# Kernel tuning notes

Measured on AMD Instinct MI355X. Metric: run time of the kernel, lower is better.

The kernel has to match this reference:

```python
import jax, jax.numpy as jnp
import numpy as np

SIGMA = 16
P = 2 * SIGMA + 1  # 33x33 patch
OUT = 128          # feature_extractor.output_size
DN = ('NCHW', 'OIHW', 'NCHW')


def setup_inputs() -> dict:
    key = jax.random.key(0)
    ks = jax.random.split(key, 10)
    B, K, H, W = 4, 64, 256, 256
    images_ground = jax.random.normal(ks[0], (B, 3, H, W), jnp.float32)
    images_satellite = jax.random.normal(ks[1], (B, 3, H, W), jnp.float32)
    # normalized keypoints kept in interior so sigma-window crops stay in-bounds
    keypoints_ground = 0.2 + 0.6 * jax.random.uniform(ks[2], (B, K, 2), jnp.float32)
    keypoints_satellite = 0.2 + 0.6 * jax.random.uniform(ks[3], (B, K, 2), jnp.float32)
    # small CNN feature extractor params (conv 3->32 s1, conv 32->64 s2, GAP, linear 64->OUT)
    w1 = jax.random.normal(ks[4], (32, 3, 3, 3), jnp.float32) * 0.1
    b1 = jnp.zeros((32,), jnp.float32)
    w2 = jax.random.normal(ks[5], (64, 32, 3, 3), jnp.float32) * 0.05
    b2 = jnp.zeros((64,), jnp.float32)
    wl = jax.random.normal(ks[6], (OUT, 64), jnp.float32) * 0.1
    bl = jnp.zeros((OUT,), jnp.float32)
    return dict(images_ground=images_ground, images_satellite=images_satellite,
                keypoints_ground=keypoints_ground, keypoints_satellite=keypoints_satellite,
                w1=w1, b1=b1, w2=w2, b2=b2, wl=wl, bl=bl, num_samples=K)


def _cnn(x, w1, b1, w2, b2, wl, bl):
    # x: [M, 3, P, P] -> [M, OUT]
    h = jax.lax.conv_general_dilated(x, w1, (1, 1), 'VALID', dimension_numbers=DN)
    h = jax.nn.relu(h + b1[None, :, None, None])
    h = jax.lax.conv_general_dilated(h, w2, (2, 2), 'VALID', dimension_numbers=DN)
    h = jax.nn.relu(h + b2[None, :, None, None])
    h = h.mean(axis=(2, 3))  # global average pool -> [M, 64]
    return h @ wl.T + bl


def _crop_all(images, kps_px):
    # images: [B,3,H,W]; kps_px: [N,2] pixel (x, y) coords -> patches [N,B,3,P,P]
    B = images.shape[0]
    hw = images.shape[-1]
    starts = jnp.clip(jnp.floor(kps_px).astype(jnp.int32) - SIGMA, 0, hw - P)
    def one(st):
        return jax.lax.dynamic_slice(images, (0, 0, st[1], st[0]), (B, 3, P, P))
    return jax.vmap(one)(starts)


def reference(images_ground, images_satellite, keypoints_ground, keypoints_satellite,
              w1, b1, w2, b2, wl, bl, num_samples):
    kg = (keypoints_ground * images_ground.shape[-1]).reshape(-1, 2)   # [N,2]
    ksat = (keypoints_satellite * images_satellite.shape[-1]).reshape(-1, 2)
    pg = _crop_all(images_ground, kg)        # [N,B,3,P,P]
    ps = _crop_all(images_satellite, ksat)   # [N,B,3,P,P]
    N, B = pg.shape[0], pg.shape[1]
    fg = _cnn(pg.reshape(N * B, 3, P, P), w1, b1, w2, b2, wl, bl)
    fs = _cnn(ps.reshape(N * B, 3, P, P), w1, b1, w2, b2, wl, bl)
    fg = fg.reshape(N, B, OUT).transpose(1, 0, 2)  # features_ground [B,N,OUT]
    fs = fs.reshape(N, B, OUT).transpose(1, 0, 2)
    return jnp.mean((fg - fs) ** 2)
```

## Files before the change

kernel.cpp:

```cpp
#include <hip/hip_runtime.h>

#define HW   256
#define Pp   33
#define PPAD 36
#define OUTF 128
#define SIG  16

#define KCP   40
#define PLROW (2 * 16 * KCP)
#define PLSZ  (6 * PLROW)
#define IMS   40

#define WS_W1FH 0
#define WS_W1FL 512
#define WS_BHI  1024
#define WS_BLO  10240
#define WS_WLT  19456

typedef __attribute__((ext_vector_type(8))) short v8s;
typedef __attribute__((ext_vector_type(4))) float f32x4;

__device__ __forceinline__ unsigned short f2bf_rne(float x) {
  unsigned u = __float_as_uint(x);
  unsigned r = (u + 0x7FFFu + ((u >> 16) & 1u)) >> 16;
  return (unsigned short)r;
}
__device__ __forceinline__ float bf2f(unsigned short h) {
  return __uint_as_float(((unsigned)h) << 16);
}

__global__ __launch_bounds__(256) void prep_kernel(
    const float* __restrict__ w1, const float* __restrict__ w2,
    const float* __restrict__ wl, float* __restrict__ ws,
    float* __restrict__ out) {
  int t = blockIdx.x * 256 + threadIdx.x;
  int stride = gridDim.x * 256;
  if (blockIdx.x == 0 && threadIdx.x == 0) out[0] = 0.0f;
  unsigned short* w1h = (unsigned short*)(ws + WS_W1FH);
  unsigned short* w1lo = (unsigned short*)(ws + WS_W1FL);
  for (int i = t; i < 1024; i += stride) {
    int j  = i & 7;
    int l  = (i >> 3) & 63;
    int nt = i >> 9;
    int k  = 8 * (l >> 4) + j;
    int ch = 16 * nt + (l & 15);
    float v = (k < 27) ? w1[ch * 27 + k] : 0.0f;
    unsigned short h = f2bf_rne(v);
    w1h[i]  = h;
    w1lo[i] = f2bf_rne(v - bf2f(h));
  }
  unsigned short* bhi = (unsigned short*)(ws + WS_BHI);
  unsigned short* blo = (unsigned short*)(ws + WS_BLO);
  for (int i = t; i < 18432; i += stride) {
    int j  = i & 7;
    int l  = (i >> 3) & 63;
    int w  = (i >> 9) & 3;
    int tp = i >> 11;
    int ch = w * 16 + (l & 15);
    int kc = ((l >> 4) << 3) + j;
    int ky = tp / 3, kx = tp - ky * 3;
    float v = w2[ch * 288 + kc * 9 + ky * 3 + kx];
    unsigned short h = f2bf_rne(v);
    bhi[i] = h;
    blo[i] = f2bf_rne(v - bf2f(h));
  }
  for (int i = t; i < 8192; i += stride) {
    int o = i & 127, ii = i >> 7;
    ws[WS_WLT + i] = wl[o * 64 + ii];
  }
}

__global__ __launch_bounds__(256) void patch_cnn_kernel(
    const float* __restrict__ imgG, const float* __restrict__ imgS,
    const float* __restrict__ kpG,  const float* __restrict__ kpS,
    const float* __restrict__ b1g,  const float* __restrict__ b2g,
    const float* __restrict__ blg,  const float* __restrict__ ws,
    float* __restrict__ out) {
  __shared__ __align__(16) unsigned short patch[3 * Pp * PPAD];
  __shared__ __align__(16) unsigned short imcol[2][32 * IMS];
  __shared__ __align__(16) unsigned short hiP[PLSZ];
  __shared__ float gapv[64];
  __shared__ float fstash[OUTF];
  __shared__ float lred[4];

  const int bid  = blockIdx.x;
  const int n    = bid >> 2;
  const int b    = bid & 3;
  const int tid  = threadIdx.x;
  const int wave = tid >> 6;
  const int lane = tid & 63;

  const int m16 = lane & 15;
  const int qq  = lane >> 4;
  const int mt  = wave & 1;
  const int nt  = wave >> 1;

  const int bm = tid & 31;
  const int kq = tid >> 5;
  int  boff[4];
  bool bval[4];
#pragma unroll
  for (int j = 0; j < 4; ++j) {
    int k = 4 * kq + j;
    bval[j] = (k < 27);
    int kk = bval[j] ? k : 0;
    int ci = kk / 9, r2 = kk - ci * 9, ky = r2 / 3, kx = r2 - ky * 3;
    boff[j] = (ci * Pp + ky) * PPAD + bm + kx;
  }

  const v8s w1hF = ((const v8s*)((const unsigned short*)(ws + WS_W1FH)))[nt * 64 + lane];
  const v8s w1lF = ((const v8s*)((const unsigned short*)(ws + WS_W1FL)))[nt * 64 + lane];
  const float b1v = b1g[nt * 16 + m16];

  const v8s* bhW = (const v8s*)((const unsigned short*)(ws + WS_BHI)) + (wave * 64 + lane);
  const v8s* blW = (const v8s*)((const unsigned short*)(ws + WS_BLO)) + (wave * 64 + lane);
  const float b2v = b2g[wave * 16 + m16];

  auto build_row = [&](int r, int ibuf) {
    unsigned short h[4];
#pragma unroll
    for (int j = 0; j < 4; ++j)
      h[j] = bval[j] ? patch[boff[j] + r * PPAD] : (unsigned short)0;
    unsigned w0 = (unsigned)h[0] | ((unsigned)h[1] << 16);
    unsigned w1_ = (unsigned)h[2] | ((unsigned)h[3] << 16);
    *(uint2*)&imcol[ibuf][bm * IMS + 4 * kq] = make_uint2(w0, w1_);
  };

  auto conv1_row = [&](int ibuf, int sl) {
    v8s af = *(const v8s*)&imcol[ibuf][(16 * mt + m16) * IMS + 8 * qq];
    f32x4 a1 = {0.f, 0.f, 0.f, 0.f};
    a1 = __builtin_amdgcn_mfma_f32_16x16x32_bf16(af, w1hF, a1, 0, 0, 0);
    a1 = __builtin_amdgcn_mfma_f32_16x16x32_bf16(af, w1lF, a1, 0, 0, 0);
#pragma unroll
    for (int rg = 0; rg < 4; ++rg) {
      int x = 16 * mt + 4 * qq + rg;
      float f = fmaxf(a1[rg] + b1v, 0.f);
      hiP[((sl * 2 + (x & 1)) * 16 + (x >> 1)) * KCP + 16 * nt + m16] = f2bf_rne(f);
    }
  };

  auto produce_pair = [&](int r0) {
    const int rB = min(r0 + 1, 30);
    int s0p = r0 % 6;
    int s1p = s0p + 1; if (s1p >= 6) s1p -= 6;
    __syncthreads();
    build_row(r0, 0);
    build_row(rB, 1);
    __syncthreads();
    conv1_row(0, s0p);
    conv1_row(1, s1p);
  };

  float dd = 0.0f;

#pragma unroll 1
  for (int side = 0; side < 2; ++side) {
    const float* img = side ? imgS : imgG;
    const float* kp  = side ? kpS : kpG;

    int sx = (int)floorf(kp[n * 2 + 0] * 256.0f) - SIG;
    int sy = (int)floorf(kp[n * 2 + 1] * 256.0f) - SIG;
    sx = min(max(sx, 0), HW - Pp);
    sy = min(max(sy, 0), HW - Pp);

    for (int i = tid; i < (3 * Pp * PPAD) / 2; i += 256) {
      int e  = 2 * i;
      int ci = e / (Pp * PPAD);
      int r2 = e - ci * (Pp * PPAD);
      int r  = r2 / PPAD;
      int cc = r2 - r * PPAD;
      float vx = 0.f, vy = 0.f;
      const float* rowp = &img[((b * 3 + ci) * HW + (sy + r)) * HW + sx];
      if (cc < 32) { float2 v = *(const float2*)(rowp + cc); vx = v.x; vy = v.y; }
      else if (cc == 32) { vx = rowp[32]; }
      unsigned pk = (unsigned)f2bf_rne(vx) | ((unsigned)f2bf_rne(vy) << 16);
      *(unsigned*)&patch[e] = pk;
    }
    produce_pair(0);
    produce_pair(2);

    float gapAcc = 0.0f;
    int s0 = 0;
#pragma unroll 1
    for (int y2 = 0; y2 < 15; ++y2) {
      __syncthreads();
      f32x4 acc = {0.f, 0.f, 0.f, 0.f};
#pragma unroll
      for (int ky = 0; ky < 3; ++ky) {
        int sk = s0 + ky; if (sk >= 6) sk -= 6;
#pragma unroll
        for (int kx = 0; kx < 3; ++kx) {
          const int p = kx & 1;
          int cp = m16 + (kx >> 1); if (cp > 15) cp = 15;
          const int idx = ((sk * 2 + p) * 16 + cp) * KCP + qq * 8;
          v8s ah = *(const v8s*)&hiP[idx];
          const int tp = ky * 3 + kx;
          v8s bh = bhW[tp * 256];
          v8s bl = blW[tp * 256];
          acc = __builtin_amdgcn_mfma_f32_16x16x32_bf16(ah, bh, acc, 0, 0, 0);
          acc = __builtin_amdgcn_mfma_f32_16x16x32_bf16(ah, bl, acc, 0, 0, 0);
        }
      }
      {
        float s = fmaxf(acc.x + b2v, 0.f) + fmaxf(acc.y + b2v, 0.f) +
                  fmaxf(acc.z + b2v, 0.f);
        if (qq < 3) s += fmaxf(acc.w + b2v, 0.f);
        gapAcc += s;
      }
      const int r0 = 2 * y2 + 4;
      if (r0 <= 30) produce_pair(r0);
      s0 += 2; if (s0 >= 6) s0 -= 6;
    }

    gapAcc += __shfl_down(gapAcc, 32, 64);
    gapAcc += __shfl_down(gapAcc, 16, 64);
    if (lane < 16) gapv[wave * 16 + m16] = gapAcc * (1.0f / 225.0f);
    __syncthreads();

    if (tid < OUTF) {
      float f = blg[tid];
#pragma unroll 8
      for (int i = 0; i < 64; ++i) f = fmaf(gapv[i], ws[WS_WLT + i * OUTF + tid], f);
      if (side == 0) fstash[tid] = f;
      else { float d = f - fstash[tid]; dd = d * d; }
    }
    __syncthreads();
  }

  dd += __shfl_down(dd, 32, 64);
  dd += __shfl_down(dd, 16, 64);
  dd += __shfl_down(dd, 8, 64);
  dd += __shfl_down(dd, 4, 64);
  dd += __shfl_down(dd, 2, 64);
  dd += __shfl_down(dd, 1, 64);
  if (lane == 0) lred[wave] = dd;
  __syncthreads();
  if (tid == 0) {
    float s = (lred[0] + lred[1]) + (lred[2] + lred[3]);
    atomicAdd(out, s * (1.0f / 131072.0f));
  }
}

extern "C" void kernel_launch(void* const* d_in, const int* in_sizes, int n_in,
                              void* d_out, int out_size, void* d_ws, size_t ws_size,
                              hipStream_t stream) {
  const float* imgG = (const float*)d_in[0];
  const float* imgS = (const float*)d_in[1];
  const float* kpG  = (const float*)d_in[2];
  const float* kpS  = (const float*)d_in[3];
  const float* w1   = (const float*)d_in[4];
  const float* b1   = (const float*)d_in[5];
  const float* w2   = (const float*)d_in[6];
  const float* b2   = (const float*)d_in[7];
  const float* wl   = (const float*)d_in[8];
  const float* bl   = (const float*)d_in[9];
  float* ws  = (float*)d_ws;
  float* out = (float*)d_out;

  hipLaunchKernelGGL(prep_kernel, dim3(32), dim3(256), 0, stream, w1, w2, wl, ws, out);
  hipLaunchKernelGGL(patch_cnn_kernel, dim3(1024), dim3(256), 0, stream,
                     imgG, imgS, kpG, kpS, b1, b2, bl, ws, out);
}
```

Before: 152.1 us.

## Software-pipeline im2col build and conv1 with conv2 using double-buffered imcol

The im2col scratch grows from two to four buffers, so the next row pair can be built while conv1 reads the current pair. Inside the row loop, conv1, the next im2col build and the conv2 MFMAs now run between a single barrier per iteration instead of three. The conv1 MFMA operands are swapped, so each lane holds four consecutive channels and writes them to hiP as one 4-short store, with the bias loaded as a float4. The cost is extra shared memory and more complex slot and buffer indexing, where any aliasing mistake would be a race.

```diff
diff --git a/kernel.cpp b/kernel.cpp
--- a/kernel.cpp
+++ b/kernel.cpp
@@ -18,6 +18,7 @@
 #define WS_WLT  19456
 
 typedef __attribute__((ext_vector_type(8))) short v8s;
+typedef __attribute__((ext_vector_type(4))) short v4s;
 typedef __attribute__((ext_vector_type(4))) float f32x4;
 
 __device__ __forceinline__ unsigned short f2bf_rne(float x) {
@@ -77,7 +78,7 @@
     const float* __restrict__ blg,  const float* __restrict__ ws,
     float* __restrict__ out) {
   __shared__ __align__(16) unsigned short patch[3 * Pp * PPAD];
-  __shared__ __align__(16) unsigned short imcol[2][32 * IMS];
+  __shared__ __align__(16) unsigned short imcol[4][32 * IMS];
   __shared__ __align__(16) unsigned short hiP[PLSZ];
   __shared__ float gapv[64];
   __shared__ float fstash[OUTF];
@@ -110,45 +111,42 @@
 
   const v8s w1hF = ((const v8s*)((const unsigned short*)(ws + WS_W1FH)))[nt * 64 + lane];
   const v8s w1lF = ((const v8s*)((const unsigned short*)(ws + WS_W1FL)))[nt * 64 + lane];
-  const float b1v = b1g[nt * 16 + m16];
+  const float4 b1q = *(const float4*)&b1g[16 * nt + 4 * qq];
 
   const v8s* bhW = (const v8s*)((const unsigned short*)(ws + WS_BHI)) + (wave * 64 + lane);
   const v8s* blW = (const v8s*)((const unsigned short*)(ws + WS_BLO)) + (wave * 64 + lane);
   const float b2v = b2g[wave * 16 + m16];
 
-  auto build_row = [&](int r, int ibuf) {
+  auto build_row = [&](int r, int d) {
     unsigned short h[4];
 #pragma unroll
     for (int j = 0; j < 4; ++j)
       h[j] = bval[j] ? patch[boff[j] + r * PPAD] : (unsigned short)0;
     unsigned w0 = (unsigned)h[0] | ((unsigned)h[1] << 16);
     unsigned w1_ = (unsigned)h[2] | ((unsigned)h[3] << 16);
-    *(uint2*)&imcol[ibuf][bm * IMS + 4 * kq] = make_uint2(w0, w1_);
+    *(uint2*)&imcol[d][bm * IMS + 4 * kq] = make_uint2(w0, w1_);
   };
 
-  auto conv1_row = [&](int ibuf, int sl) {
-    v8s af = *(const v8s*)&imcol[ibuf][(16 * mt + m16) * IMS + 8 * qq];
-    f32x4 a1 = {0.f, 0.f, 0.f, 0.f};
-    a1 = __builtin_amdgcn_mfma_f32_16x16x32_bf16(af, w1hF, a1, 0, 0, 0);
-    a1 = __builtin_amdgcn_mfma_f32_16x16x32_bf16(af, w1lF, a1, 0, 0, 0);
-#pragma unroll
-    for (int rg = 0; rg < 4; ++rg) {
-      int x = 16 * mt + 4 * qq + rg;
-      float f = fmaxf(a1[rg] + b1v, 0.f);
-      hiP[((sl * 2 + (x & 1)) * 16 + (x >> 1)) * KCP + 16 * nt + m16] = f2bf_rne(f);
-    }
-  };
-
-  auto produce_pair = [&](int r0) {
-    const int rB = min(r0 + 1, 30);
-    int s0p = r0 % 6;
-    int s1p = s0p + 1; if (s1p >= 6) s1p -= 6;
-    __syncthreads();
-    build_row(r0, 0);
-    build_row(rB, 1);
-    __syncthreads();
-    conv1_row(0, s0p);
-    conv1_row(1, s1p);
+  auto conv1_pair = [&](int bp, int r0) {
+#pragma unroll
+    for (int rr = 0; rr < 2; ++rr) {
+      const int row = r0 + rr;
+      if (row <= 30) {
+        int sl = row % 6;
+        v8s af = *(const v8s*)&imcol[2 * bp + rr][(16 * mt + m16) * IMS + 8 * qq];
+        f32x4 a1 = {0.f, 0.f, 0.f, 0.f};
+        a1 = __builtin_amdgcn_mfma_f32_16x16x32_bf16(w1hF, af, a1, 0, 0, 0);
+        a1 = __builtin_amdgcn_mfma_f32_16x16x32_bf16(w1lF, af, a1, 0, 0, 0);
+        const int x = 16 * mt + m16;
+        v4s hv;
+        hv[0] = (short)f2bf_rne(fmaxf(a1.x + b1q.x, 0.f));
+        hv[1] = (short)f2bf_rne(fmaxf(a1.y + b1q.y, 0.f));
+        hv[2] = (short)f2bf_rne(fmaxf(a1.z + b1q.z, 0.f));
+        hv[3] = (short)f2bf_rne(fmaxf(a1.w + b1q.w, 0.f));
+        const int idx = ((sl * 2 + (x & 1)) * 16 + (x >> 1)) * KCP + 16 * nt + 4 * qq;
+        *(v4s*)&hiP[idx] = hv;
+      }
+    }
   };
 
   float dd = 0.0f;
@@ -176,14 +174,27 @@
       unsigned pk = (unsigned)f2bf_rne(vx) | ((unsigned)f2bf_rne(vy) << 16);
       *(unsigned*)&patch[e] = pk;
     }
-    produce_pair(0);
-    produce_pair(2);
+    __syncthreads();
+
+    build_row(0, 0); build_row(1, 1);
+    __syncthreads();
+    conv1_pair(0, 0); build_row(2, 2); build_row(3, 3);
+    __syncthreads();
+    conv1_pair(1, 2); build_row(4, 0); build_row(5, 1);
+    __syncthreads();
 
     float gapAcc = 0.0f;
     int s0 = 0;
+    int bp = 0;
 #pragma unroll 1
     for (int y2 = 0; y2 < 15; ++y2) {
-      __syncthreads();
+      const int r0 = 2 * y2 + 4;
+      if (r0 <= 30) conv1_pair(bp, r0);
+      const int r1 = 2 * y2 + 6;
+      if (r1 <= 30) {
+        build_row(r1, 2 * (bp ^ 1));
+        build_row(min(r1 + 1, 30), 2 * (bp ^ 1) + 1);
+      }
       f32x4 acc = {0.f, 0.f, 0.f, 0.f};
 #pragma unroll
       for (int ky = 0; ky < 3; ++ky) {
@@ -207,9 +218,9 @@
         if (qq < 3) s += fmaxf(acc.w + b2v, 0.f);
         gapAcc += s;
       }
-      const int r0 = 2 * y2 + 4;
-      if (r0 <= 30) produce_pair(r0);
+      __syncthreads();
       s0 += 2; if (s0 >= 6) s0 -= 6;
+      bp ^= 1;
     }
 
     gapAcc += __shfl_down(gapAcc, 32, 64);
```

Result: no change. 152.5 us (+0.2%).
